# Kernel optimization log

Measured on AMD Instinct MI355X. Metric: run time of the kernel, lower is better.

Reference implementation:

```python
import jax, jax.numpy as jnp
import numpy as np
import math

B, S, D, H = 2, 2048, 512, 8
DK = D // H  # 64
NEG_INF = float('-inf')


def setup_inputs() -> dict:
    key = jax.random.key(0)
    ks = jax.random.split(key, 16)
    s = 1.0 / math.sqrt(D)
    return {
        'in_Q': jax.random.normal(ks[0], (B, S, D), jnp.float32),
        'in_K': jax.random.normal(ks[1], (B, S, D), jnp.float32),
        'in_V': jax.random.normal(ks[2], (B, S, D), jnp.float32),
        'row_pad_mask': jax.random.randint(ks[3], (B, S), 0, 2, jnp.int32),
        'col_pad_mask': jax.random.randint(ks[4], (B, S), 0, 2, jnp.int32),
        'W_Q': jax.random.uniform(ks[5], (D, D), jnp.float32, -s, s),
        'b_Q': jax.random.uniform(ks[6], (D,), jnp.float32, -s, s),
        'W_K': jax.random.uniform(ks[7], (D, D), jnp.float32, -s, s),
        'b_K': jax.random.uniform(ks[8], (D,), jnp.float32, -s, s),
        'W_V': jax.random.uniform(ks[9], (D, D), jnp.float32, -s, s),
        'b_V': jax.random.uniform(ks[10], (D,), jnp.float32, -s, s),
        'W_O': jax.random.uniform(ks[11], (D, D), jnp.float32, -s, s),
        'b_O': jax.random.uniform(ks[12], (D,), jnp.float32, -s, s),
    }


def reference(in_Q, in_K, in_V, row_pad_mask, col_pad_mask,
              W_Q, b_Q, W_K, b_K, W_V, b_V, W_O, b_O):
    b, sq, _ = in_Q.shape
    sk = in_K.shape[1]
    # projections (torch Linear: x @ W.T + b)
    Q = in_Q @ W_Q.T + b_Q
    K = in_K @ W_K.T + b_K
    V = in_V @ W_V.T + b_V
    # chunk along feature dim + stack == reshape to heads: [b, h, s, dk]
    Qh = Q.reshape(b, sq, H, DK).transpose(0, 2, 1, 3)
    Kh = K.reshape(b, sk, H, DK).transpose(0, 2, 1, 3)
    Vh = V.reshape(b, sk, H, DK).transpose(0, 2, 1, 3)
    scores = jnp.einsum('bhqd,bhkd->bhqk', Qh, Kh) / math.sqrt(DK)
    # causal mask (additive -inf above diagonal, as in the original)
    causal = jnp.triu(jnp.full((sq, sk), NEG_INF, scores.dtype), k=1)
    scores = scores + causal
    # padding masks: pad masks encode lengths via their row sums
    row_len = row_pad_mask.sum(axis=1)  # [b]
    col_len = col_pad_mask.sum(axis=1)
    row_np = jnp.arange(sq)[None, :] < row_len[:, None]  # [b, sq]
    col_np = jnp.arange(sk)[None, :] < col_len[:, None]  # [b, sk]
    non_pad = (row_np[:, :, None] & col_np[:, None, :])[:, None]  # [b,1,sq,sk]
    scores = jnp.where(non_pad, scores, NEG_INF)
    p = jax.nn.softmax(scores, axis=-1)
    p = jnp.nan_to_num(p)  # fully-masked rows -> 0 (matches torch nan_to_num)
    attn = jnp.einsum('bhqk,bhkd->bhqd', p, Vh)
    Hcat = attn.transpose(0, 2, 1, 3).reshape(b, sq, D)
    return Hcat @ W_O.T + b_O
```

## Files before the change

### kernel.cpp

```cpp
#include <hip/hip_runtime.h>

#define S_LEN 2048
#define D_MODEL 512
#define NHEAD 8
#define BATCH 2

typedef __attribute__((ext_vector_type(8))) short bf16x8;
typedef __attribute__((ext_vector_type(4))) float f32x4;

__device__ __forceinline__ unsigned short f2bf(float f) {
    union { float f; unsigned u; } v; v.f = f;
    unsigned u = v.u + 0x7FFFu + ((v.u >> 16) & 1u);
    return (unsigned short)(u >> 16);
}

__device__ __forceinline__ void gl_lds16(const unsigned short* g, unsigned short* l) {
    __builtin_amdgcn_global_load_lds(
        (const __attribute__((address_space(1))) void*)g,
        (__attribute__((address_space(3))) void*)l,
        16, 0, 0);
}

__global__ __launch_bounds__(256) void cvtlens_kernel(
    const float* __restrict__ inQ, const float* __restrict__ inK, const float* __restrict__ inV,
    const float* __restrict__ WQ, const float* __restrict__ WK,
    const float* __restrict__ WV, const float* __restrict__ WO,
    const int* __restrict__ rpm, const int* __restrict__ cpm,
    unsigned short* __restrict__ Xbf, unsigned short* __restrict__ Wbf,
    int* __restrict__ lens)
{
    const int t = threadIdx.x;
    if (blockIdx.x < 2) {
        __shared__ int red[256];
        const int b = blockIdx.x;
        int sr = 0, sc2 = 0;
        for (int i = t; i < S_LEN; i += 256) {
            sr  += rpm[b * S_LEN + i];
            sc2 += cpm[b * S_LEN + i];
        }
        red[t] = sr;
        __syncthreads();
        for (int off = 128; off > 0; off >>= 1) {
            if (t < off) red[t] += red[t + off];
            __syncthreads();
        }
        if (t == 0) lens[b * 2 + 0] = red[0];
        __syncthreads();
        red[t] = sc2;
        __syncthreads();
        for (int off = 128; off > 0; off >>= 1) {
            if (t < off) red[t] += red[t + off];
            __syncthreads();
        }
        if (t == 0) lens[b * 2 + 1] = red[0];
    }

    const int NXC = 786432;
    const int NTOT = 917504;
    const int stride = gridDim.x * 256;
    for (int c = blockIdx.x * 256 + t; c < NTOT; c += stride) {
        if (c < NXC) {
            const int flat = c << 3;
            const int z = flat >> 21;
            const int off = flat & 2097151;
            const float* src = ((z == 0) ? inQ : (z == 1) ? inK : inV) + off;
            float4 a = *(const float4*)src;
            float4 d = *(const float4*)(src + 4);
            unsigned short* w = Xbf + flat;
            w[0] = f2bf(a.x); w[1] = f2bf(a.y); w[2] = f2bf(a.z); w[3] = f2bf(a.w);
            w[4] = f2bf(d.x); w[5] = f2bf(d.y); w[6] = f2bf(d.z); w[7] = f2bf(d.w);
        } else {
            const int wflat = (c - NXC) << 3;
            const int wz = wflat >> 18;
            const int off = wflat & 262143;
            const float* src = ((wz == 0) ? WQ : (wz == 1) ? WK : (wz == 2) ? WV : WO) + off;
            float4 a = *(const float4*)src;
            float4 d = *(const float4*)(src + 4);
            unsigned short* w = Wbf + wflat;
            w[0] = f2bf(a.x); w[1] = f2bf(a.y); w[2] = f2bf(a.z); w[3] = f2bf(a.w);
            w[4] = f2bf(d.x); w[5] = f2bf(d.y); w[6] = f2bf(d.z); w[7] = f2bf(d.w);
        }
    }
}

__global__ __launch_bounds__(256) void proj_gemm(
    const unsigned short* __restrict__ Xbf, const unsigned short* __restrict__ Wbf,
    const float* __restrict__ bQ, const float* __restrict__ bK, const float* __restrict__ bV,
    const int* __restrict__ lens,
    unsigned short* __restrict__ Qg, unsigned short* __restrict__ Kg,
    unsigned short* __restrict__ VTg)
{
    __shared__ __align__(16) unsigned short Xld[128 * 32];
    __shared__ __align__(16) unsigned short Wld[128 * 32];

    const int z = blockIdx.z;
    const int tileS = blockIdx.x * 128;
    const int tileF = blockIdx.y * 128;
    const int bb0 = tileS >> 11;
    const int rl = lens[bb0 * 2], cl = lens[bb0 * 2 + 1];
    const int limit = (z == 0) ? rl : cl;
    if ((tileS & 2047) >= limit) return;

    const unsigned short* X = Xbf + (size_t)z * (4096 * 512);
    const unsigned short* W = Wbf + (size_t)z * (512 * 512);
    const float* bias = (z == 0) ? bQ : (z == 1) ? bK : bV;

    const int t = threadIdx.x;
    const int wv = t >> 6, lane = t & 63, l15 = lane & 15, quad = lane >> 4;
    const int srow = t >> 2, scq = t & 3;
    const int c_sw = scq ^ ((srow >> 1) & 3);

    const unsigned short* gX = X + (size_t)(tileS + srow) * 512 + c_sw * 8;
    const unsigned short* gW = W + (size_t)(tileF + srow) * 512 + c_sw * 8;
    unsigned short* lX0 = Xld + wv * 512;
    unsigned short* lW0 = Wld + wv * 512;

    const int f_off = (wv & 1) * 64, s_off = (wv >> 1) * 64;

    f32x4 acc[4][4] = {};

    for (int kk = 0; kk < 16; ++kk) {
        if (kk) __syncthreads();
        const int k0 = kk * 32;
        gl_lds16(gX + k0,            lX0);
        gl_lds16(gX + k0 + 64 * 512, lX0 + 2048);
        gl_lds16(gW + k0,            lW0);
        gl_lds16(gW + k0 + 64 * 512, lW0 + 2048);
        __syncthreads();
        bf16x8 wf[4], xf[4];
        #pragma unroll
        for (int i = 0; i < 4; ++i) {
            const int rw = f_off + i * 16 + l15;
            wf[i] = *(const bf16x8*)(Wld + rw * 32 + (quad ^ ((rw >> 1) & 3)) * 8);
            const int rx = s_off + i * 16 + l15;
            xf[i] = *(const bf16x8*)(Xld + rx * 32 + (quad ^ ((rx >> 1) & 3)) * 8);
        }
        #pragma unroll
        for (int ft = 0; ft < 4; ++ft)
            #pragma unroll
            for (int st = 0; st < 4; ++st)
                acc[ft][st] = __builtin_amdgcn_mfma_f32_16x16x32_bf16(
                    wf[ft], xf[st], acc[ft][st], 0, 0, 0);
    }

    #pragma unroll
    for (int ft = 0; ft < 4; ++ft) {
        const int f = tileF + f_off + ft * 16 + quad * 4;
        const int h = f >> 6, dk = f & 63;
        const float b0 = bias[f], b1 = bias[f + 1], b2 = bias[f + 2], b3 = bias[f + 3];
        #pragma unroll
        for (int st = 0; st < 4; ++st) {
            const int s = tileS + s_off + st * 16 + l15;
            const int bb = s >> 11, seq = s & 2047;
            const f32x4 a = acc[ft][st];
            if (z <= 1) {
                unsigned short* dst = ((z == 0) ? Qg : Kg)
                    + ((size_t)((bb * 8 + h) * 2048 + seq)) * 64 + dk;
                ushort4 u;
                u.x = f2bf(a[0] + b0); u.y = f2bf(a[1] + b1);
                u.z = f2bf(a[2] + b2); u.w = f2bf(a[3] + b3);
                *(ushort4*)dst = u;
            } else {
                unsigned short* dst = VTg
                    + ((size_t)((bb * 8 + h) * 64 + dk)) * 2048 + seq;
                dst[0]    = f2bf(a[0] + b0);
                dst[2048] = f2bf(a[1] + b1);
                dst[4096] = f2bf(a[2] + b2);
                dst[6144] = f2bf(a[3] + b3);
            }
        }
    }
}

__global__ __launch_bounds__(256) void attn_kernel(
    const unsigned short* __restrict__ Qg, const unsigned short* __restrict__ Kg,
    const unsigned short* __restrict__ VTg, const int* __restrict__ lens,
    unsigned short* __restrict__ AO)
{
    __shared__ __align__(16) unsigned short Pl[4 * 16 * 72];
    __shared__ __align__(16) float Po[4 * 16 * 68];
    __shared__ float Ml[4 * 16];
    __shared__ float Ll[4 * 16];

    const int t = threadIdx.x;
    const int wv = t >> 6, lane = t & 63, l15 = lane & 15, quad = lane >> 4;
    const int bh = blockIdx.y;
    const int b = bh >> 3, h = bh & 7;
    const int q0 = blockIdx.x * 16;
    const int rl = lens[b * 2], cl = lens[b * 2 + 1];

    if (q0 >= rl) {
        const int row = t >> 4, cg = t & 15;
        ushort4 zz = {0, 0, 0, 0};
        *(ushort4*)(AO + ((size_t)(b * 2048 + q0 + row)) * 512 + h * 64 + cg * 4) = zz;
        return;
    }

    const unsigned short* Qrow = Qg + ((size_t)(bh * 2048 + q0 + l15)) * 64;
    const bf16x8 aq0 = *(const bf16x8*)(Qrow + quad * 8);
    const bf16x8 aq1 = *(const bf16x8*)(Qrow + 32 + quad * 8);

    unsigned short* pb = Pl + wv * (16 * 72);

    f32x4 oacc[4] = {};
    float m_[4], l_[4];
    #pragma unroll
    for (int r = 0; r < 4; ++r) { m_[r] = -__builtin_inff(); l_[r] = 0.f; }

    const int q_end = q0 + 16;
    const int kv_max = (cl < q_end) ? cl : q_end;
    const int ntiles = (kv_max + 63) >> 6;
    const int qrow0 = q0 + quad * 4;

    for (int kt = wv; kt < ntiles; kt += 4) {
        const int kv0 = kt * 64;
        f32x4 sc[4] = {};
        #pragma unroll
        for (int ct = 0; ct < 4; ++ct) {
            const unsigned short* Krow = Kg + ((size_t)(bh * 2048 + kv0 + ct * 16 + l15)) * 64;
            sc[ct] = __builtin_amdgcn_mfma_f32_16x16x32_bf16(
                aq0, *(const bf16x8*)(Krow + quad * 8), sc[ct], 0, 0, 0);
            sc[ct] = __builtin_amdgcn_mfma_f32_16x16x32_bf16(
                aq1, *(const bf16x8*)(Krow + 32 + quad * 8), sc[ct], 0, 0, 0);
        }

        const bool full = (kv0 + 64 <= q0) && (kv0 + 64 <= cl) && (q_end <= rl);

        #pragma unroll
        for (int r = 0; r < 4; ++r) {
            const int q = qrow0 + r;
            float mx = -__builtin_inff();
            if (full) {
                #pragma unroll
                for (int ct = 0; ct < 4; ++ct) {
                    const float s = sc[ct][r] * 0.125f;
                    sc[ct][r] = s;
                    mx = fmaxf(mx, s);
                }
            } else {
                #pragma unroll
                for (int ct = 0; ct < 4; ++ct) {
                    const int kv = kv0 + ct * 16 + l15;
                    float s = sc[ct][r] * 0.125f;
                    const bool valid = (q < rl) && (kv < cl) && (kv <= q);
                    s = valid ? s : -__builtin_inff();
                    sc[ct][r] = s;
                    mx = fmaxf(mx, s);
                }
            }
            mx = fmaxf(mx, __shfl_xor(mx, 1, 16));
            mx = fmaxf(mx, __shfl_xor(mx, 2, 16));
            mx = fmaxf(mx, __shfl_xor(mx, 4, 16));
            mx = fmaxf(mx, __shfl_xor(mx, 8, 16));

            const float mold = m_[r];
            const float mnew = fmaxf(mold, mx);
            const float alpha = (mold == -__builtin_inff()) ? 0.f : __expf(mold - mnew);
            float psum = 0.f;
            #pragma unroll
            for (int ct = 0; ct < 4; ct++) {
                const float sv = sc[ct][r];
                const float p = (mnew == -__builtin_inff()) ? 0.f : __expf(sv - mnew);
                sc[ct][r] = p;
                psum += p;
            }
            psum += __shfl_xor(psum, 1, 16);
            psum += __shfl_xor(psum, 2, 16);
            psum += __shfl_xor(psum, 4, 16);
            psum += __shfl_xor(psum, 8, 16);
            l_[r] = alpha * l_[r] + psum;
            m_[r] = mnew;
            #pragma unroll
            for (int ct = 0; ct < 4; ct++) oacc[ct][r] *= alpha;
        }

        #pragma unroll
        for (int ct = 0; ct < 4; ++ct) {
            #pragma unroll
            for (int r = 0; r < 4; ++r)
                pb[(quad * 4 + r) * 72 + ct * 16 + l15] = f2bf(sc[ct][r]);
        }
        const bf16x8 pf0 = *(const bf16x8*)(pb + l15 * 72 + quad * 8);
        const bf16x8 pf1 = *(const bf16x8*)(pb + l15 * 72 + 32 + quad * 8);
        #pragma unroll
        for (int ct = 0; ct < 4; ++ct) {
            const unsigned short* Vrow = VTg + ((size_t)(bh * 64 + ct * 16 + l15)) * 2048 + kv0;
            oacc[ct] = __builtin_amdgcn_mfma_f32_16x16x32_bf16(
                pf0, *(const bf16x8*)(Vrow + quad * 8), oacc[ct], 0, 0, 0);
            oacc[ct] = __builtin_amdgcn_mfma_f32_16x16x32_bf16(
                pf1, *(const bf16x8*)(Vrow + 32 + quad * 8), oacc[ct], 0, 0, 0);
        }
    }

    #pragma unroll
    for (int ct = 0; ct < 4; ++ct) {
        #pragma unroll
        for (int r = 0; r < 4; ++r)
            Po[wv * 1088 + (quad * 4 + r) * 68 + ct * 16 + l15] = oacc[ct][r];
    }
    if (l15 == 0) {
        #pragma unroll
        for (int r = 0; r < 4; ++r) {
            Ml[wv * 16 + quad * 4 + r] = m_[r];
            Ll[wv * 16 + quad * 4 + r] = l_[r];
        }
    }
    __syncthreads();

    const int row = t >> 4, cg = t & 15;
    float mw[4];
    float mstar = -__builtin_inff();
    #pragma unroll
    for (int w = 0; w < 4; ++w) {
        mw[w] = Ml[w * 16 + row];
        mstar = fmaxf(mstar, mw[w]);
    }
    f32x4 o = {};
    if (mstar != -__builtin_inff()) {
        float lst = 0.f;
        #pragma unroll
        for (int w = 0; w < 4; ++w) {
            const float sw = (mw[w] == -__builtin_inff()) ? 0.f : __expf(mw[w] - mstar);
            lst += sw * Ll[w * 16 + row];
            const f32x4 pv = *(const f32x4*)&Po[w * 1088 + row * 68 + cg * 4];
            o[0] += sw * pv[0]; o[1] += sw * pv[1];
            o[2] += sw * pv[2]; o[3] += sw * pv[3];
        }
        const float inv = (lst > 0.f) ? 1.f / lst : 0.f;
        o[0] *= inv; o[1] *= inv; o[2] *= inv; o[3] *= inv;
    }
    ushort4 u;
    u.x = f2bf(o[0]); u.y = f2bf(o[1]); u.z = f2bf(o[2]); u.w = f2bf(o[3]);
    *(ushort4*)(AO + ((size_t)(b * 2048 + q0 + row)) * 512 + h * 64 + cg * 4) = u;
}

__global__ __launch_bounds__(256) void out_gemm(
    const unsigned short* __restrict__ AO, const unsigned short* __restrict__ Wbf,
    const float* __restrict__ bO, const int* __restrict__ lens, float* __restrict__ out)
{
    __shared__ __align__(16) unsigned short Xld[128 * 32];
    __shared__ __align__(16) unsigned short Wld[128 * 32];

    const int tileS = blockIdx.x * 128;
    const int tileF = blockIdx.y * 128;
    const int bb0 = tileS >> 11;
    const int rl = lens[bb0 * 2];
    const int t = threadIdx.x;

    if ((tileS & 2047) >= rl) {
        const int r0 = t >> 2;
        const int cg = (t & 3) * 32;
        float4 bv[8];
        #pragma unroll
        for (int j = 0; j < 8; ++j) bv[j] = *(const float4*)(bO + tileF + cg + j * 4);
        #pragma unroll
        for (int i = 0; i < 2; ++i) {
            float* orow = out + (size_t)(tileS + i * 64 + r0) * 512 + tileF + cg;
            #pragma unroll
            for (int j = 0; j < 8; ++j) *(float4*)(orow + j * 4) = bv[j];
        }
        return;
    }

    const unsigned short* W = Wbf + (size_t)3 * (512 * 512);
    const int wv = t >> 6, lane = t & 63, l15 = lane & 15, quad = lane >> 4;
    const int srow = t >> 2, scq = t & 3;
    const int c_sw = scq ^ ((srow >> 1) & 3);

    const unsigned short* gX = AO + (size_t)(tileS + srow) * 512 + c_sw * 8;
    const unsigned short* gW = W + (size_t)(tileF + srow) * 512 + c_sw * 8;
    unsigned short* lX0 = Xld + wv * 512;
    unsigned short* lW0 = Wld + wv * 512;

    const int f_off = (wv & 1) * 64, s_off = (wv >> 1) * 64;

    f32x4 acc[4][4] = {};

    for (int kk = 0; kk < 16; ++kk) {
        if (kk) __syncthreads();
        const int k0 = kk * 32;
        gl_lds16(gX + k0,            lX0);
        gl_lds16(gX + k0 + 64 * 512, lX0 + 2048);
        gl_lds16(gW + k0,            lW0);
        gl_lds16(gW + k0 + 64 * 512, lW0 + 2048);
        __syncthreads();
        bf16x8 wf[4], xf[4];
        #pragma unroll
        for (int i = 0; i < 4; ++i) {
            const int rw = f_off + i * 16 + l15;
            wf[i] = *(const bf16x8*)(Wld + rw * 32 + (quad ^ ((rw >> 1) & 3)) * 8);
            const int rx = s_off + i * 16 + l15;
            xf[i] = *(const bf16x8*)(Xld + rx * 32 + (quad ^ ((rx >> 1) & 3)) * 8);
        }
        #pragma unroll
        for (int ft = 0; ft < 4; ++ft)
            #pragma unroll
            for (int st = 0; st < 4; ++st)
                acc[ft][st] = __builtin_amdgcn_mfma_f32_16x16x32_bf16(
                    wf[ft], xf[st], acc[ft][st], 0, 0, 0);
    }

    #pragma unroll
    for (int ft = 0; ft < 4; ++ft) {
        const int f = tileF + f_off + ft * 16 + quad * 4;
        const float4 bv = *(const float4*)(bO + f);
        #pragma unroll
        for (int st = 0; st < 4; ++st) {
            const int s = tileS + s_off + st * 16 + l15;
            float4 o;
            o.x = acc[ft][st][0] + bv.x;
            o.y = acc[ft][st][1] + bv.y;
            o.z = acc[ft][st][2] + bv.z;
            o.w = acc[ft][st][3] + bv.w;
            *(float4*)(out + (size_t)s * 512 + f) = o;
        }
    }
}

extern "C" void kernel_launch(void* const* d_in, const int* in_sizes, int n_in,
                              void* d_out, int out_size, void* d_ws, size_t ws_size,
                              hipStream_t stream)
{
    const float* inQ = (const float*)d_in[0];
    const float* inK = (const float*)d_in[1];
    const float* inV = (const float*)d_in[2];
    const int*   rpm = (const int*)d_in[3];
    const int*   cpm = (const int*)d_in[4];
    const float* WQ  = (const float*)d_in[5];
    const float* bQ  = (const float*)d_in[6];
    const float* WK  = (const float*)d_in[7];
    const float* bK  = (const float*)d_in[8];
    const float* WV  = (const float*)d_in[9];
    const float* bV  = (const float*)d_in[10];
    const float* WO  = (const float*)d_in[11];
    const float* bO  = (const float*)d_in[12];
    float* out = (float*)d_out;

    char* ws = (char*)d_ws;
    unsigned short* Xbf = (unsigned short*)(ws);
    unsigned short* Wbf = (unsigned short*)(ws + 12582912);
    unsigned short* Qg  = (unsigned short*)(ws + 14680064);
    unsigned short* Kg  = (unsigned short*)(ws + 18874368);
    unsigned short* VTg = (unsigned short*)(ws + 23068672);
    unsigned short* AO  = (unsigned short*)(ws + 27262976);
    int* lens           = (int*)(ws + 31457280);

    cvtlens_kernel<<<dim3(1792), dim3(256), 0, stream>>>(
        inQ, inK, inV, WQ, WK, WV, WO, rpm, cpm, Xbf, Wbf, lens);
    proj_gemm<<<dim3(32, 4, 3), dim3(256), 0, stream>>>(
        Xbf, Wbf, bQ, bK, bV, lens, Qg, Kg, VTg);
    attn_kernel<<<dim3(128, 16), dim3(256), 0, stream>>>(Qg, Kg, VTg, lens, AO);
    out_gemm<<<dim3(32, 4), dim3(256), 0, stream>>>(AO, Wbf, bO, lens, out);
}
```

Before: 162.5 us.

## Double GEMM K-tile to 64 with new LDS swizzle; fold softmax scale into Q

Both projection and output GEMMs now stage 64-wide K slices per iteration instead of 32. This halves the barrier count and the number of loop trips, and uses a new XOR swizzle over 8 chunks so LDS reads avoid bank conflicts. The 1/sqrt(dk) scale is applied to Q when it is written in the projection epilogue, which removes the per-score multiply in the attention softmax. LDS use per block doubles, and pre-scaling Q before the bf16 rounding slightly changes the numerics.

```diff
diff --git a/kernel.cpp b/kernel.cpp
--- a/kernel.cpp
+++ b/kernel.cpp
@@ -90,8 +90,8 @@
     unsigned short* __restrict__ Qg, unsigned short* __restrict__ Kg,
     unsigned short* __restrict__ VTg)
 {
-    __shared__ __align__(16) unsigned short Xld[128 * 32];
-    __shared__ __align__(16) unsigned short Wld[128 * 32];
+    __shared__ __align__(16) unsigned short Xld[128 * 64];
+    __shared__ __align__(16) unsigned short Wld[128 * 64];
 
     const int z = blockIdx.z;
     const int tileS = blockIdx.x * 128;
@@ -107,42 +107,48 @@
 
     const int t = threadIdx.x;
     const int wv = t >> 6, lane = t & 63, l15 = lane & 15, quad = lane >> 4;
-    const int srow = t >> 2, scq = t & 3;
-    const int c_sw = scq ^ ((srow >> 1) & 3);
-
-    const unsigned short* gX = X + (size_t)(tileS + srow) * 512 + c_sw * 8;
-    const unsigned short* gW = W + (size_t)(tileF + srow) * 512 + c_sw * 8;
-    unsigned short* lX0 = Xld + wv * 512;
-    unsigned short* lW0 = Wld + wv * 512;
+    const int ro = lane >> 3;
+    const int lc8 = ((lane & 7) ^ ro) * 8;
+
+    const unsigned short* gX = X + (size_t)(tileS + wv * 32 + ro) * 512 + lc8;
+    const unsigned short* gW = W + (size_t)(tileF + wv * 32 + ro) * 512 + lc8;
+    unsigned short* lX0 = Xld + wv * 2048;
+    unsigned short* lW0 = Wld + wv * 2048;
 
     const int f_off = (wv & 1) * 64, s_off = (wv >> 1) * 64;
+    const int swk = l15 & 7;
 
     f32x4 acc[4][4] = {};
 
-    for (int kk = 0; kk < 16; ++kk) {
+    for (int kk = 0; kk < 8; ++kk) {
         if (kk) __syncthreads();
-        const int k0 = kk * 32;
-        gl_lds16(gX + k0,            lX0);
-        gl_lds16(gX + k0 + 64 * 512, lX0 + 2048);
-        gl_lds16(gW + k0,            lW0);
-        gl_lds16(gW + k0 + 64 * 512, lW0 + 2048);
+        const int k0 = kk * 64;
+        #pragma unroll
+        for (int j = 0; j < 4; ++j) {
+            gl_lds16(gX + j * 8 * 512 + k0, lX0 + j * 512);
+            gl_lds16(gW + j * 8 * 512 + k0, lW0 + j * 512);
+        }
         __syncthreads();
-        bf16x8 wf[4], xf[4];
-        #pragma unroll
-        for (int i = 0; i < 4; ++i) {
-            const int rw = f_off + i * 16 + l15;
-            wf[i] = *(const bf16x8*)(Wld + rw * 32 + (quad ^ ((rw >> 1) & 3)) * 8);
-            const int rx = s_off + i * 16 + l15;
-            xf[i] = *(const bf16x8*)(Xld + rx * 32 + (quad ^ ((rx >> 1) & 3)) * 8);
-        }
-        #pragma unroll
-        for (int ft = 0; ft < 4; ++ft)
-            #pragma unroll
-            for (int st = 0; st < 4; ++st)
-                acc[ft][st] = __builtin_amdgcn_mfma_f32_16x16x32_bf16(
-                    wf[ft], xf[st], acc[ft][st], 0, 0, 0);
-    }
-
+        #pragma unroll
+        for (int kk2 = 0; kk2 < 2; ++kk2) {
+            bf16x8 wf[4], xf[4];
+            #pragma unroll
+            for (int i = 0; i < 4; ++i) {
+                const int rw = f_off + i * 16 + l15;
+                wf[i] = *(const bf16x8*)(Wld + rw * 64 + ((kk2 * 4 + quad) ^ swk) * 8);
+                const int rx = s_off + i * 16 + l15;
+                xf[i] = *(const bf16x8*)(Xld + rx * 64 + ((kk2 * 4 + quad) ^ swk) * 8);
+            }
+            #pragma unroll
+            for (int ft = 0; ft < 4; ++ft)
+                #pragma unroll
+                for (int st = 0; st < 4; ++st)
+                    acc[ft][st] = __builtin_amdgcn_mfma_f32_16x16x32_bf16(
+                        wf[ft], xf[st], acc[ft][st], 0, 0, 0);
+        }
+    }
+
+    const float oscale = (z == 0) ? 0.125f : 1.0f;
     #pragma unroll
     for (int ft = 0; ft < 4; ++ft) {
         const int f = tileF + f_off + ft * 16 + quad * 4;
@@ -157,8 +163,8 @@
                 unsigned short* dst = ((z == 0) ? Qg : Kg)
                     + ((size_t)((bb * 8 + h) * 2048 + seq)) * 64 + dk;
                 ushort4 u;
-                u.x = f2bf(a[0] + b0); u.y = f2bf(a[1] + b1);
-                u.z = f2bf(a[2] + b2); u.w = f2bf(a[3] + b3);
+                u.x = f2bf((a[0] + b0) * oscale); u.y = f2bf((a[1] + b1) * oscale);
+                u.z = f2bf((a[2] + b2) * oscale); u.w = f2bf((a[3] + b3) * oscale);
                 *(ushort4*)dst = u;
             } else {
                 unsigned short* dst = VTg
@@ -232,16 +238,12 @@
             float mx = -__builtin_inff();
             if (full) {
                 #pragma unroll
-                for (int ct = 0; ct < 4; ++ct) {
-                    const float s = sc[ct][r] * 0.125f;
-                    sc[ct][r] = s;
-                    mx = fmaxf(mx, s);
-                }
+                for (int ct = 0; ct < 4; ++ct) mx = fmaxf(mx, sc[ct][r]);
             } else {
                 #pragma unroll
                 for (int ct = 0; ct < 4; ++ct) {
                     const int kv = kv0 + ct * 16 + l15;
-                    float s = sc[ct][r] * 0.125f;
+                    float s = sc[ct][r];
                     const bool valid = (q < rl) && (kv < cl) && (kv <= q);
                     s = valid ? s : -__builtin_inff();
                     sc[ct][r] = s;
@@ -338,8 +340,8 @@
     const unsigned short* __restrict__ AO, const unsigned short* __restrict__ Wbf,
     const float* __restrict__ bO, const int* __restrict__ lens, float* __restrict__ out)
 {
-    __shared__ __align__(16) unsigned short Xld[128 * 32];
-    __shared__ __align__(16) unsigned short Wld[128 * 32];
+    __shared__ __align__(16) unsigned short Xld[128 * 64];
+    __shared__ __align__(16) unsigned short Wld[128 * 64];
 
     const int tileS = blockIdx.x * 128;
     const int tileF = blockIdx.y * 128;
@@ -364,40 +366,45 @@
 
     const unsigned short* W = Wbf + (size_t)3 * (512 * 512);
     const int wv = t >> 6, lane = t & 63, l15 = lane & 15, quad = lane >> 4;
-    const int srow = t >> 2, scq = t & 3;
-    const int c_sw = scq ^ ((srow >> 1) & 3);
-
-    const unsigned short* gX = AO + (size_t)(tileS + srow) * 512 + c_sw * 8;
-    const unsigned short* gW = W + (size_t)(tileF + srow) * 512 + c_sw * 8;
-    unsigned short* lX0 = Xld + wv * 512;
-    unsigned short* lW0 = Wld + wv * 512;
+    const int ro = lane >> 3;
+    const int lc8 = ((lane & 7) ^ ro) * 8;
+
+    const unsigned short* gX = AO + (size_t)(tileS + wv * 32 + ro) * 512 + lc8;
+    const unsigned short* gW = W + (size_t)(tileF + wv * 32 + ro) * 512 + lc8;
+    unsigned short* lX0 = Xld + wv * 2048;
+    unsigned short* lW0 = Wld + wv * 2048;
 
     const int f_off = (wv & 1) * 64, s_off = (wv >> 1) * 64;
+    const int swk = l15 & 7;
 
     f32x4 acc[4][4] = {};
 
-    for (int kk = 0; kk < 16; ++kk) {
+    for (int kk = 0; kk < 8; ++kk) {
         if (kk) __syncthreads();
-        const int k0 = kk * 32;
-        gl_lds16(gX + k0,            lX0);
-        gl_lds16(gX + k0 + 64 * 512, lX0 + 2048);
-        gl_lds16(gW + k0,            lW0);
-        gl_lds16(gW + k0 + 64 * 512, lW0 + 2048);
+        const int k0 = kk * 64;
+        #pragma unroll
+        for (int j = 0; j < 4; ++j) {
+            gl_lds16(gX + j * 8 * 512 + k0, lX0 + j * 512);
+            gl_lds16(gW + j * 8 * 512 + k0, lW0 + j * 512);
+        }
         __syncthreads();
-        bf16x8 wf[4], xf[4];
-        #pragma unroll
-        for (int i = 0; i < 4; ++i) {
-            const int rw = f_off + i * 16 + l15;
-            wf[i] = *(const bf16x8*)(Wld + rw * 32 + (quad ^ ((rw >> 1) & 3)) * 8);
-            const int rx = s_off + i * 16 + l15;
-            xf[i] = *(const bf16x8*)(Xld + rx * 32 + (quad ^ ((rx >> 1) & 3)) * 8);
-        }
-        #pragma unroll
-        for (int ft = 0; ft < 4; ++ft)
-            #pragma unroll
-            for (int st = 0; st < 4; ++st)
-                acc[ft][st] = __builtin_amdgcn_mfma_f32_16x16x32_bf16(
-                    wf[ft], xf[st], acc[ft][st], 0, 0, 0);
+        #pragma unroll
+        for (int kk2 = 0; kk2 < 2; ++kk2) {
+            bf16x8 wf[4], xf[4];
+            #pragma unroll
+            for (int i = 0; i < 4; ++i) {
+                const int rw = f_off + i * 16 + l15;
+                wf[i] = *(const bf16x8*)(Wld + rw * 64 + ((kk2 * 4 + quad) ^ swk) * 8);
+                const int rx = s_off + i * 16 + l15;
+                xf[i] = *(const bf16x8*)(Xld + rx * 64 + ((kk2 * 4 + quad) ^ swk) * 8);
+            }
+            #pragma unroll
+            for (int ft = 0; ft < 4; ++ft)
+                #pragma unroll
+                for (int st = 0; st < 4; ++st)
+                    acc[ft][st] = __builtin_amdgcn_mfma_f32_16x16x32_bf16(
+                        wf[ft], xf[st], acc[ft][st], 0, 0, 0);
+        }
     }
 
     #pragma unroll
```

Result: faster. 158.0 us (-2.8%).
